# Performance work log

Measured on AMD Instinct MI355X. Metric: run time of the kernel, lower is better.

Reference implementation:

```python
import jax, jax.numpy as jnp
import numpy as np

B, S, D = 1, 2048, 2048      # batch, seq, hidden_dim
DF = 768                      # moe intermediate (per routed expert)
DSH = 2048                    # shared-expert intermediate
E, K = 32, 8                  # num routed experts, top_k
BLK = 128                     # fp8 block-scale size
CAP = 1024
T = B * S


def _dequant(w, s, blk=BLK):
    # w: [E, M, N] fp8 values (stored fp32), s: [E, M/blk, N/blk] block scales
    Eh, M, N = w.shape
    Mb, Nb = s.shape[1], s.shape[2]
    return (w.reshape(Eh, Mb, blk, Nb, blk) * s[:, :, None, :, None]).reshape(Eh, M, N)


def setup_inputs() -> dict:
    key = jax.random.key(0)
    ks = jax.random.split(key, 13)
    n = lambda k, shp, sc=0.02: jax.random.normal(k, shp, jnp.float32) * sc
    u = lambda k, shp: jax.random.uniform(k, shp, jnp.float32, 0.005, 0.02)
    return {
        "hidden_states": jax.random.normal(ks[0], (B, S, D), jnp.float32),
        "router_w": n(ks[1], (E, D)),
        # raw fp8-value weights (simulated as fp32 integers-in-range values) + block scale_inv
        "wg_fp8": jax.random.normal(ks[2], (E, DF, D), jnp.float32),
        "sg": u(ks[3], (E, DF // BLK, D // BLK)),
        "wu_fp8": jax.random.normal(ks[4], (E, DF, D), jnp.float32),
        "su": u(ks[5], (E, DF // BLK, D // BLK)),
        "wd_fp8": jax.random.normal(ks[6], (E, D, DF), jnp.float32),
        "sd": u(ks[7], (E, D // BLK, DF // BLK)),
        "ws_gate": n(ks[8], (DSH, D)),
        "ws_up": n(ks[9], (DSH, D)),
        "ws_down": n(ks[10], (D, DSH)),
        "w_shared_gate": n(ks[11], (1, D)),
    }


def reference(hidden_states, router_w, wg_fp8, sg, wu_fp8, su, wd_fp8, sd,
              ws_gate, ws_up, ws_down, w_shared_gate):
    x = hidden_states.reshape(-1, D)  # [T, D]

    # shared expert (SwiGLU) + its sigmoid gate
    shared = (jax.nn.silu(x @ ws_gate.T) * (x @ ws_up.T)) @ ws_down.T
    sh_gate = jax.nn.sigmoid(x @ w_shared_gate.T)  # [T, 1]

    # router: softmax -> top-k -> renormalize (Qwen MoE gate)
    probs = jax.nn.softmax(x @ router_w.T, axis=-1)          # [T, E]
    rw, sel = jax.lax.top_k(probs, K)                        # [T, K]
    rw = rw / jnp.sum(rw, axis=-1, keepdims=True)

    # capacity-based dispatch (replaces the python per-expert loop; same math)
    flat_e = sel.reshape(-1)                                 # [T*K]
    oh = jax.nn.one_hot(flat_e, E, dtype=jnp.int32)
    pos = jnp.sum(jnp.cumsum(oh, axis=0) * oh, axis=-1) - 1  # position within expert
    keep = (pos < CAP)
    pos_c = jnp.minimum(pos, CAP)                            # overflow -> scratch slot CAP
    tok = jnp.arange(T * K) // K                             # owning token of each (t,k) pair

    buf = jnp.zeros((E, CAP + 1, D), x.dtype).at[flat_e, pos_c].set(x[tok])

    # block-scale dequant (fp8*scale_inv), then per-expert SwiGLU
    Wg = _dequant(wg_fp8, sg)
    Wu = _dequant(wu_fp8, su)
    Wd = _dequant(wd_fp8, sd)
    g = jnp.einsum('ecd,efd->ecf', buf, Wg)
    up = jnp.einsum('ecd,efd->ecf', buf, Wu)
    h = jax.nn.silu(g) * up
    y = jnp.einsum('ecf,edf->ecd', h, Wd)                    # [E, CAP+1, D]

    # weighted scatter-add back to tokens (index_add_ equivalent)
    y_tok = y[flat_e, pos_c]                                 # [T*K, D]
    w_tok = rw.reshape(-1) * keep.astype(x.dtype)
    out = jax.ops.segment_sum(y_tok * w_tok[:, None], tok, num_segments=T)

    out = out + sh_gate * shared
    return out.reshape(B, S, D)
```

## Files before the change

### kernel.cpp

```cpp
#include <hip/hip_runtime.h>
#include <hip/hip_bf16.h>


#define TT   2048
#define DD   2048
#define DFF  768
#define DSH  2048
#define EE   32
#define KTOP 8
#define CAP  1024

typedef _Float16 half8  __attribute__((ext_vector_type(8)));
typedef _Float16 half4v __attribute__((ext_vector_type(4)));
typedef float    f32x4  __attribute__((ext_vector_type(4)));

__global__ __launch_bounds__(256) void k_init(int* __restrict__ cnt,
                                              int* __restrict__ slot_tok) {
  int i = blockIdx.x * 256 + threadIdx.x;
  if (i < EE * CAP) slot_tok[i] = 0;
  if (i < EE) cnt[i] = 0;
}

__global__ __launch_bounds__(256) void k_zero(float* __restrict__ out) {
  int i = blockIdx.x * 256 + threadIdx.x;
  ((float4*)out)[i] = (float4){0.f, 0.f, 0.f, 0.f};
}

__global__ __launch_bounds__(256) void k_cast(const float* __restrict__ in,
                                              _Float16* __restrict__ out) {
  int i = blockIdx.x * 256 + threadIdx.x;
  float4 v = ((const float4*)in)[i];
  half4v h = { (_Float16)v.x, (_Float16)v.y, (_Float16)v.z, (_Float16)v.w };
  ((half4v*)out)[i] = h;
}

__global__ __launch_bounds__(64) void k_router(
    const float* __restrict__ x, const float* __restrict__ rw,
    const float* __restrict__ wshg,
    float* __restrict__ shg, int* __restrict__ cnt,
    int* __restrict__ slot_tok, float* __restrict__ slot_w) {
  int t = blockIdx.x;
  int lane = threadIdx.x;
  const float* xr = x + (size_t)t * DD;
  float xv[32];
#pragma unroll
  for (int j = 0; j < 32; ++j) xv[j] = xr[lane + j * 64];

  __shared__ float lg[EE];
  for (int e = 0; e < EE; ++e) {
    const float* we = rw + (size_t)e * DD;
    float s = 0.f;
#pragma unroll
    for (int j = 0; j < 32; ++j) s += xv[j] * we[lane + j * 64];
#pragma unroll
    for (int off = 32; off > 0; off >>= 1) s += __shfl_down(s, off);
    if (lane == 0) lg[e] = s;
  }
  {
    float s = 0.f;
#pragma unroll
    for (int j = 0; j < 32; ++j) s += xv[j] * wshg[lane + j * 64];
#pragma unroll
    for (int off = 32; off > 0; off >>= 1) s += __shfl_down(s, off);
    if (lane == 0) shg[t] = 1.f / (1.f + expf(-s));
  }
  if (lane == 0) {
    unsigned used = 0;
    int sel[KTOP];
    float val[KTOP];
    for (int k = 0; k < KTOP; ++k) {
      float bv = -1e30f; int bi = 0;
      for (int e = 0; e < EE; ++e)
        if (!((used >> e) & 1) && lg[e] > bv) { bv = lg[e]; bi = e; }
      used |= (1u << bi);
      sel[k] = bi; val[k] = bv;
    }
    float mx = val[0], sum = 0.f;
    for (int k = 0; k < KTOP; ++k) { val[k] = expf(val[k] - mx); sum += val[k]; }
    float inv = 1.f / sum;
    for (int k = 0; k < KTOP; ++k) {
      int e = sel[k];
      int pos = atomicAdd(&cnt[e], 1);
      if (pos < CAP) {
        slot_tok[e * CAP + pos] = t;
        slot_w[e * CAP + pos] = val[k] * inv;
      }
    }
  }
}

template<bool DUAL, bool GATHER, bool DEQ, int EPI, int NPB, int MBB, int KDIM>
__global__ __launch_bounds__(256, 2) void k_gemm(
    const _Float16* __restrict__ A,
    const float* __restrict__ B0f, const float* __restrict__ B1f,
    const float* __restrict__ S0, const float* __restrict__ S1,
    int sCols, int sStrideE,
    _Float16* __restrict__ OutH, float* __restrict__ OutF,
    const float* __restrict__ shg,
    int ldA, int ldOut,
    long long strideAE, long long strideBE, long long strideOE,
    const int* __restrict__ cnt, int rowsConst,
    const int* __restrict__ slot_tok, const float* __restrict__ slot_w) {
  constexpr int BK = 64;
  constexpr int KT = KDIM / BK;
  constexpr int NF = DUAL ? 2 : 4;
  constexpr int BN = DUAL ? 64 : 128;
  constexpr int BCH = DUAL ? 4 : 8;

  const int f = blockIdx.x;
  const int xcd = f & 7;
  const int t0 = f >> 3;
  const int mb = t0 % MBB;
  const int pp = t0 / MBB;
  const int p  = pp * 8 + xcd;
  const int nb = p % NPB;
  const int e  = p / NPB;

  int rows = cnt ? (cnt[e] > CAP ? CAP : cnt[e]) : rowsConst;
  const int rowBase = mb * 128;
  if (rowBase >= rows) return;
  const int nBase = nb * BN;

  const int tid = threadIdx.x;
  const int lane = tid & 63;
  const int wave = tid >> 6;
  const int wr = wave >> 1;
  const int wc = wave & 1;

  __shared__ __align__(16) _Float16 sA[3][8192];
  __shared__ __align__(16) _Float16 sB[2][8192];

  const _Float16* Ae = A + (GATHER ? 0 : (long long)e * strideAE);
  const float* B0e = B0f + (long long)e * strideBE;
  const float* B1e = DUAL ? (B1f + (long long)e * strideBE) : nullptr;
  const float* S0e = DEQ ? (S0 + (long long)e * sStrideE) : nullptr;
  const float* S1e = (DEQ && DUAL) ? (S1 + (long long)e * sStrideE) : nullptr;
  const int sRow = DEQ ? (nBase >> 7) * sCols : 0;

  long long aByte[4];
#pragma unroll
  for (int i = 0; i < 4; ++i) {
    int c = tid + i * 256;
    int row = c >> 3;
    int colB = ((c & 7) << 4) ^ ((row & 7) << 4);
    int src = GATHER ? slot_tok[e * CAP + rowBase + row] : (rowBase + row);
    aByte[i] = (long long)src * (2LL * ldA) + colB;
  }
  long long bOff[BCH];
  int wByte[BCH];
#pragma unroll
  for (int i = 0; i < BCH; ++i) {
    int c = tid + i * 256;
    int rn = c >> 4;
    int c4 = (c & 15) << 2;
    bOff[i] = (long long)(nBase + rn) * KDIM + c4;
    wByte[i] = ((rn << 7) + (c4 << 1)) ^ ((rn & 7) << 4);
  }

  f32x4 accG[4][NF];
  f32x4 accU[DUAL ? 4 : 1][NF];
#pragma unroll
  for (int m = 0; m < 4; ++m)
#pragma unroll
    for (int n = 0; n < NF; ++n) {
      accG[m][n] = (f32x4){0.f, 0.f, 0.f, 0.f};
      if constexpr (DUAL) accU[m][n] = (f32x4){0.f, 0.f, 0.f, 0.f};
    }

  auto stageA = [&](int kt, int buf) {
#pragma unroll
    for (int i = 0; i < 4; ++i) {
      __builtin_amdgcn_global_load_lds(
          (const __attribute__((address_space(1))) void*)
              ((const char*)Ae + aByte[i] + kt * (BK * 2)),
          (__attribute__((address_space(3))) void*)&sA[buf][(size_t)(tid + i * 256) * 8],
          16, 0, 0);
    }
  };
  auto loadB = [&](int kt, float4 (&r0)[BCH], float4 (&r1)[BCH]) {
    const int ko = kt * BK;
#pragma unroll
    for (int i = 0; i < BCH; ++i) r0[i] = *(const float4*)(B0e + bOff[i] + ko);
    if constexpr (DUAL) {
#pragma unroll
      for (int i = 0; i < BCH; ++i) r1[i] = *(const float4*)(B1e + bOff[i] + ko);
    }
  };
  auto storeB = [&](int kt, float4 (&r0)[BCH], float4 (&r1)[BCH]) {
    float s0 = 1.f, s1 = 1.f;
    if constexpr (DEQ) {
      s0 = S0e[sRow + (kt >> 1)];
      if constexpr (DUAL) s1 = S1e[sRow + (kt >> 1)];
    }
    char* base = (char*)&sB[kt & 1][0];
#pragma unroll
    for (int i = 0; i < BCH; ++i) {
      half4v h = { (_Float16)(r0[i].x * s0), (_Float16)(r0[i].y * s0),
                   (_Float16)(r0[i].z * s0), (_Float16)(r0[i].w * s0) };
      *(half4v*)(base + wByte[i]) = h;
      if constexpr (DUAL) {
        half4v h1 = { (_Float16)(r1[i].x * s1), (_Float16)(r1[i].y * s1),
                      (_Float16)(r1[i].z * s1), (_Float16)(r1[i].w * s1) };
        *(half4v*)(base + 8192 + wByte[i]) = h1;
      }
    }
  };
  auto computeTile = [&](int ia, int ib) {
    const char* pA = (const char*)&sA[ia][0];
    const char* pB = (const char*)&sB[ib][0];
#pragma unroll
    for (int kk = 0; kk < 2; ++kk) {
      const int koff = kk * 32 + (lane >> 4) * 8;
      half8 a[4];
#pragma unroll
      for (int m = 0; m < 4; ++m) {
        int r = wr * 64 + m * 16 + (lane & 15);
        int byt = ((r << 7) + (koff << 1)) ^ ((r & 7) << 4);
        a[m] = *(const half8*)(pA + byt);
      }
      if constexpr (DUAL) {
        half8 bg[2], bu[2];
#pragma unroll
        for (int n = 0; n < 2; ++n) {
          int rn = wc * 32 + n * 16 + (lane & 15);
          int byt = ((rn << 7) + (koff << 1)) ^ ((rn & 7) << 4);
          bg[n] = *(const half8*)(pB + byt);
          bu[n] = *(const half8*)(pB + 8192 + byt);
        }
#pragma unroll
        for (int m = 0; m < 4; ++m)
#pragma unroll
          for (int n = 0; n < 2; ++n) {
            accG[m][n] = __builtin_amdgcn_mfma_f32_16x16x32_f16(a[m], bg[n], accG[m][n], 0, 0, 0);
            accU[m][n] = __builtin_amdgcn_mfma_f32_16x16x32_f16(a[m], bu[n], accU[m][n], 0, 0, 0);
          }
      } else {
        half8 b[4];
#pragma unroll
        for (int n = 0; n < 4; ++n) {
          int rn = wc * 64 + n * 16 + (lane & 15);
          int byt = ((rn << 7) + (koff << 1)) ^ ((rn & 7) << 4);
          b[n] = *(const half8*)(pB + byt);
        }
#pragma unroll
        for (int m = 0; m < 4; ++m)
#pragma unroll
          for (int n = 0; n < 4; ++n)
            accG[m][n] = __builtin_amdgcn_mfma_f32_16x16x32_f16(a[m], b[n], accG[m][n], 0, 0, 0);
      }
    }
  };

  float4 rbE0[BCH], rbE1[BCH], rbO0[BCH], rbO1[BCH];

  stageA(0, 0); loadB(0, rbE0, rbE1);
  __builtin_amdgcn_sched_barrier(0);
  stageA(1, 1); loadB(1, rbO0, rbO1);
  __builtin_amdgcn_sched_barrier(0);

  int bufC = 0;
  int bufW = 2;

  for (int kt = 0; kt < KT; kt += 2) {
    if (kt + 1 < KT) { asm volatile("s_waitcnt vmcnt(12)" ::: "memory"); }
    else             { asm volatile("s_waitcnt vmcnt(0)"  ::: "memory"); }
    __builtin_amdgcn_sched_barrier(0);
    storeB(kt, rbE0, rbE1);
    asm volatile("s_waitcnt lgkmcnt(0)" ::: "memory");
    __builtin_amdgcn_sched_barrier(0);
    __builtin_amdgcn_s_barrier();
    __builtin_amdgcn_sched_barrier(0);
    if (kt + 2 < KT) { stageA(kt + 2, bufW); loadB(kt + 2, rbE0, rbE1); }
    __builtin_amdgcn_sched_barrier(0);
    computeTile(bufC, 0);
    bufC = (bufC == 2) ? 0 : bufC + 1;
    bufW = (bufW == 2) ? 0 : bufW + 1;

    if (kt + 2 < KT) { asm volatile("s_waitcnt vmcnt(12)" ::: "memory"); }
    else             { asm volatile("s_waitcnt vmcnt(0)"  ::: "memory"); }
    __builtin_amdgcn_sched_barrier(0);
    storeB(kt + 1, rbO0, rbO1);
    asm volatile("s_waitcnt lgkmcnt(0)" ::: "memory");
    __builtin_amdgcn_sched_barrier(0);
    __builtin_amdgcn_s_barrier();
    __builtin_amdgcn_sched_barrier(0);
    if (kt + 3 < KT) { stageA(kt + 3, bufW); loadB(kt + 3, rbO0, rbO1); }
    __builtin_amdgcn_sched_barrier(0);
    computeTile(bufC, 1);
    bufC = (bufC == 2) ? 0 : bufC + 1;
    bufW = (bufW == 2) ? 0 : bufW + 1;
  }

#pragma unroll
  for (int m = 0; m < 4; ++m) {
#pragma unroll
    for (int i = 0; i < 4; ++i) {
      int row = rowBase + wr * 64 + m * 16 + (lane >> 4) * 4 + i;
      if (row < rows) {
        if constexpr (EPI == 1) {
          int tok = slot_tok[e * CAP + row];
          float w = slot_w[e * CAP + row];
#pragma unroll
          for (int n = 0; n < NF; ++n) {
            int col = nBase + wc * 64 + n * 16 + (lane & 15);
            unsafeAtomicAdd(&OutF[(long long)tok * DD + col], w * accG[m][n][i]);
          }
        } else if constexpr (EPI == 2) {
          float g = shg[row];
#pragma unroll
          for (int n = 0; n < NF; ++n) {
            int col = nBase + wc * 64 + n * 16 + (lane & 15);
            long long o = (long long)row * DD + col;
            OutF[o] += g * accG[m][n][i];
          }
        } else {
          long long outBase = (long long)e * strideOE;
#pragma unroll
          for (int n = 0; n < NF; ++n) {
            int col = nBase + (DUAL ? wc * 32 : wc * 64) + n * 16 + (lane & 15);
            long long o = outBase + (long long)row * ldOut + col;
            if constexpr (DUAL) {
              float gv = accG[m][n][i];
              float uv = accU[m][n][i];
              OutH[o] = (_Float16)((gv / (1.f + __expf(-gv))) * uv);
            } else {
              OutH[o] = (_Float16)accG[m][n][i];
            }
          }
        }
      }
    }
  }
}

extern "C" void kernel_launch(void* const* d_in, const int* in_sizes, int n_in,
                              void* d_out, int out_size, void* d_ws, size_t ws_size,
                              hipStream_t stream) {
  (void)in_sizes; (void)n_in; (void)out_size; (void)ws_size;
  const float* x    = (const float*)d_in[0];
  const float* rw   = (const float*)d_in[1];
  const float* wg   = (const float*)d_in[2];
  const float* sg   = (const float*)d_in[3];
  const float* wu   = (const float*)d_in[4];
  const float* su   = (const float*)d_in[5];
  const float* wd   = (const float*)d_in[6];
  const float* sd   = (const float*)d_in[7];
  const float* wsg  = (const float*)d_in[8];
  const float* wsu  = (const float*)d_in[9];
  const float* wsd  = (const float*)d_in[10];
  const float* wshg = (const float*)d_in[11];
  float* out = (float*)d_out;

  char* p = (char*)d_ws;
  auto alloc = [&](size_t bytes) {
    char* r = p;
    p += (bytes + 255) & ~(size_t)255;
    return r;
  };
  _Float16* x_h = (_Float16*)alloc((size_t)TT * DD * 2);
  _Float16* H   = (_Float16*)alloc((size_t)EE * CAP * DFF * 2);
  _Float16* Hsh = (_Float16*)alloc((size_t)TT * DSH * 2);
  float* shg    = (float*)alloc((size_t)TT * 4);
  int* cnt      = (int*)alloc((size_t)EE * 4);
  int* slot_tok = (int*)alloc((size_t)EE * CAP * 4);
  float* slot_w = (float*)alloc((size_t)EE * CAP * 4);

  k_init<<<(EE * CAP + 255) / 256, 256, 0, stream>>>(cnt, slot_tok);
  k_zero<<<(TT * DD / 4) / 256, 256, 0, stream>>>(out);
  k_cast<<<(TT * DD / 4) / 256, 256, 0, stream>>>(x, x_h);
  k_router<<<TT, 64, 0, stream>>>(x, rw, wshg, shg, cnt, slot_tok, slot_w);

  k_gemm<true, true, true, 0, 12, 8, DD><<<3072, 256, 0, stream>>>(
      x_h, wg, wu, sg, su, DD / 128, (DFF / 128) * (DD / 128),
      H, nullptr, nullptr,
      DD, DFF,
      0LL, (long long)DFF * DD, (long long)CAP * DFF,
      cnt, 0, slot_tok, nullptr);

  k_gemm<false, false, true, 1, 16, 8, DFF><<<4096, 256, 0, stream>>>(
      H, wd, wd, sd, sd, DFF / 128, (DD / 128) * (DFF / 128),
      nullptr, out, nullptr,
      DFF, DD,
      (long long)CAP * DFF, (long long)DD * DFF, 0LL,
      cnt, 0, slot_tok, slot_w);

  k_gemm<true, false, false, 0, 32, 16, DD><<<512, 256, 0, stream>>>(
      x_h, wsg, wsu, nullptr, nullptr, 0, 0,
      Hsh, nullptr, nullptr,
      DD, DSH,
      0LL, 0LL, 0LL,
      nullptr, TT, nullptr, nullptr);

  k_gemm<false, false, false, 2, 16, 16, DSH><<<256, 256, 0, stream>>>(
      Hsh, wsd, wsd, nullptr, nullptr, 0, 0,
      nullptr, out, shg,
      DSH, DD,
      0LL, 0LL, 0LL,
      nullptr, TT, nullptr, nullptr);
}
```

Measured before the change: 708.6 us.

## Use 512-thread 256-row GEMM tiles with phased LDS pipeline and cached scales

```diff
diff --git a/kernel.cpp b/kernel.cpp
--- a/kernel.cpp
+++ b/kernel.cpp
@@ -90,11 +90,11 @@
 }
 
 template<bool DUAL, bool GATHER, bool DEQ, int EPI, int NPB, int MBB, int KDIM>
-__global__ __launch_bounds__(256, 2) void k_gemm(
+__global__ __launch_bounds__(512, 2) void k_gemm(
     const _Float16* __restrict__ A,
     const float* __restrict__ B0f, const float* __restrict__ B1f,
     const float* __restrict__ S0, const float* __restrict__ S1,
-    int sCols, int sStrideE,
+    int sStrideE,
     _Float16* __restrict__ OutH, float* __restrict__ OutF,
     const float* __restrict__ shg,
     int ldA, int ldOut,
@@ -103,9 +103,8 @@
     const int* __restrict__ slot_tok, const float* __restrict__ slot_w) {
   constexpr int BK = 64;
   constexpr int KT = KDIM / BK;
-  constexpr int NF = DUAL ? 2 : 4;
-  constexpr int BN = DUAL ? 64 : 128;
-  constexpr int BCH = DUAL ? 4 : 8;
+  constexpr int KS = KDIM / 128;
+  constexpr int NFE = DUAL ? 1 : 2;
 
   const int f = blockIdx.x;
   const int xcd = f & 7;
@@ -117,215 +116,217 @@
   const int e  = p / NPB;
 
   int rows = cnt ? (cnt[e] > CAP ? CAP : cnt[e]) : rowsConst;
-  const int rowBase = mb * 128;
+  const int rowBase = mb * 256;
   if (rowBase >= rows) return;
-  const int nBase = nb * BN;
+  const int nBase = nb * (DUAL ? 64 : 128);
 
   const int tid = threadIdx.x;
   const int lane = tid & 63;
   const int wave = tid >> 6;
-  const int wr = wave >> 1;
-  const int wc = wave & 1;
-
-  __shared__ __align__(16) _Float16 sA[3][8192];
+  const int wr = wave >> 2;
+  const int wc = wave & 3;
+
+  __shared__ __align__(16) _Float16 sA[3][16384];
   __shared__ __align__(16) _Float16 sB[2][8192];
+  __shared__ float sSc[2][16];
 
   const _Float16* Ae = A + (GATHER ? 0 : (long long)e * strideAE);
   const float* B0e = B0f + (long long)e * strideBE;
   const float* B1e = DUAL ? (B1f + (long long)e * strideBE) : nullptr;
-  const float* S0e = DEQ ? (S0 + (long long)e * sStrideE) : nullptr;
-  const float* S1e = (DEQ && DUAL) ? (S1 + (long long)e * sStrideE) : nullptr;
-  const int sRow = DEQ ? (nBase >> 7) * sCols : 0;
-
-  long long aByte[4];
+
+  if constexpr (DEQ) {
+    const int sRow = (nBase >> 7) * KS;
+    if (tid < KS) sSc[0][tid] = S0[(long long)e * sStrideE + sRow + tid];
+    if (DUAL && tid >= 64 && tid < 64 + KS)
+      sSc[1][tid - 64] = S1[(long long)e * sStrideE + sRow + tid - 64];
+    __syncthreads();
+  }
+
+  int aByte[4];
 #pragma unroll
   for (int i = 0; i < 4; ++i) {
-    int c = tid + i * 256;
+    int c = tid + i * 512;
     int row = c >> 3;
     int colB = ((c & 7) << 4) ^ ((row & 7) << 4);
     int src = GATHER ? slot_tok[e * CAP + rowBase + row] : (rowBase + row);
-    aByte[i] = (long long)src * (2LL * ldA) + colB;
-  }
-  long long bOff[BCH];
-  int wByte[BCH];
-#pragma unroll
-  for (int i = 0; i < BCH; ++i) {
-    int c = tid + i * 256;
-    int rn = c >> 4;
-    int c4 = (c & 15) << 2;
-    bOff[i] = (long long)(nBase + rn) * KDIM + c4;
-    wByte[i] = ((rn << 7) + (c4 << 1)) ^ ((rn & 7) << 4);
-  }
-
-  f32x4 accG[4][NF];
-  f32x4 accU[DUAL ? 4 : 1][NF];
-#pragma unroll
-  for (int m = 0; m < 4; ++m)
-#pragma unroll
-    for (int n = 0; n < NF; ++n) {
-      accG[m][n] = (f32x4){0.f, 0.f, 0.f, 0.f};
-      if constexpr (DUAL) accU[m][n] = (f32x4){0.f, 0.f, 0.f, 0.f};
-    }
+    aByte[i] = src * (2 * ldA) + colB;
+  }
+  int bOff[4], wByte[4];
+#pragma unroll
+  for (int i = 0; i < 4; ++i) {
+    int c = tid + i * 512;
+    int rn = DUAL ? ((c & 1023) >> 4) : (c >> 4);
+    int c4 = (c & 15) * 4;
+    bOff[i] = (nBase + rn) * KDIM + c4;
+    wByte[i] = ((DUAL && i >= 2) ? 8192 : 0) +
+               ((((rn << 7) + (c4 << 1)) ^ ((rn & 7) << 4)));
+  }
+
+  f32x4 accG[8][NFE];
+  f32x4 accU[DUAL ? 8 : 1][1];
+#pragma unroll
+  for (int m = 0; m < 8; ++m) {
+#pragma unroll
+    for (int n = 0; n < NFE; ++n) accG[m][n] = (f32x4){0.f, 0.f, 0.f, 0.f};
+    if constexpr (DUAL) accU[m][0] = (f32x4){0.f, 0.f, 0.f, 0.f};
+  }
 
   auto stageA = [&](int kt, int buf) {
 #pragma unroll
     for (int i = 0; i < 4; ++i) {
       __builtin_amdgcn_global_load_lds(
           (const __attribute__((address_space(1))) void*)
-              ((const char*)Ae + aByte[i] + kt * (BK * 2)),
-          (__attribute__((address_space(3))) void*)&sA[buf][(size_t)(tid + i * 256) * 8],
+              ((const char*)Ae + (long long)aByte[i] + kt * 128),
+          (__attribute__((address_space(3))) void*)&sA[buf][(tid + i * 512) * 8],
           16, 0, 0);
     }
   };
-  auto loadB = [&](int kt, float4 (&r0)[BCH], float4 (&r1)[BCH]) {
+  auto loadB = [&](int kt, float4 (&r)[4]) {
     const int ko = kt * BK;
 #pragma unroll
-    for (int i = 0; i < BCH; ++i) r0[i] = *(const float4*)(B0e + bOff[i] + ko);
-    if constexpr (DUAL) {
-#pragma unroll
-      for (int i = 0; i < BCH; ++i) r1[i] = *(const float4*)(B1e + bOff[i] + ko);
+    for (int i = 0; i < 4; ++i) {
+      const float* src = (DUAL && i >= 2) ? B1e : B0e;
+      r[i] = *(const float4*)(src + bOff[i] + ko);
     }
   };
-  auto storeB = [&](int kt, float4 (&r0)[BCH], float4 (&r1)[BCH]) {
+  auto writeB = [&](int tw, float4 (&r)[4]) {
     float s0 = 1.f, s1 = 1.f;
     if constexpr (DEQ) {
-      s0 = S0e[sRow + (kt >> 1)];
-      if constexpr (DUAL) s1 = S1e[sRow + (kt >> 1)];
-    }
-    char* base = (char*)&sB[kt & 1][0];
-#pragma unroll
-    for (int i = 0; i < BCH; ++i) {
-      half4v h = { (_Float16)(r0[i].x * s0), (_Float16)(r0[i].y * s0),
-                   (_Float16)(r0[i].z * s0), (_Float16)(r0[i].w * s0) };
+      s0 = sSc[0][tw >> 1];
+      if constexpr (DUAL) s1 = sSc[1][tw >> 1];
+    }
+    char* base = (char*)&sB[0][0] + (tw & 1) * 16384;
+#pragma unroll
+    for (int i = 0; i < 4; ++i) {
+      float sc = (DUAL && i >= 2) ? s1 : s0;
+      half4v h = { (_Float16)(r[i].x * sc), (_Float16)(r[i].y * sc),
+                   (_Float16)(r[i].z * sc), (_Float16)(r[i].w * sc) };
       *(half4v*)(base + wByte[i]) = h;
-      if constexpr (DUAL) {
-        half4v h1 = { (_Float16)(r1[i].x * s1), (_Float16)(r1[i].y * s1),
-                      (_Float16)(r1[i].z * s1), (_Float16)(r1[i].w * s1) };
-        *(half4v*)(base + 8192 + wByte[i]) = h1;
-      }
     }
   };
-  auto computeTile = [&](int ia, int ib) {
-    const char* pA = (const char*)&sA[ia][0];
-    const char* pB = (const char*)&sB[ib][0];
-#pragma unroll
-    for (int kk = 0; kk < 2; ++kk) {
-      const int koff = kk * 32 + (lane >> 4) * 8;
-      half8 a[4];
-#pragma unroll
-      for (int m = 0; m < 4; ++m) {
-        int r = wr * 64 + m * 16 + (lane & 15);
-        int byt = ((r << 7) + (koff << 1)) ^ ((r & 7) << 4);
-        a[m] = *(const half8*)(pA + byt);
-      }
-      if constexpr (DUAL) {
-        half8 bg[2], bu[2];
-#pragma unroll
-        for (int n = 0; n < 2; ++n) {
-          int rn = wc * 32 + n * 16 + (lane & 15);
-          int byt = ((rn << 7) + (koff << 1)) ^ ((rn & 7) << 4);
-          bg[n] = *(const half8*)(pB + byt);
-          bu[n] = *(const half8*)(pB + 8192 + byt);
+
+  float4 rE[4], rO[4];
+
+  loadB(0, rE); stageA(0, 0);
+  loadB(1, rO); stageA(1, 1);
+  asm volatile("s_waitcnt vmcnt(12)" ::: "memory");
+  writeB(0, rE);
+  asm volatile("s_waitcnt lgkmcnt(0)" ::: "memory");
+  __builtin_amdgcn_sched_barrier(0);
+  __builtin_amdgcn_s_barrier();
+
+  const int koffB0 = (lane >> 4) * 16;
+
+  auto tile = [&](int t, int bufR, int bufD, float4 (&rIss)[4], float4 (&rWr)[4]) {
+    const char* pA = (const char*)&sA[0][0] + bufR * 32768;
+    const char* pB = (const char*)&sB[0][0] + (t & 1) * 16384;
+    half8 bg[2], bu[2], bs0[2], bs1[2];
+#pragma unroll
+    for (int ph = 0; ph < 4; ++ph) {
+      if (ph == 0) {
+        if (t + 2 < KT) loadB(t + 2, rIss);
+        if constexpr (DUAL) {
+          int rn = wc * 16 + (lane & 15);
+          int rb = rn << 7, sw = (rn & 7) << 4;
+          bg[0] = *(const half8*)(pB + ((rb + koffB0) ^ sw));
+          bg[1] = *(const half8*)(pB + ((rb + koffB0 + 64) ^ sw));
+          bu[0] = *(const half8*)(pB + 8192 + ((rb + koffB0) ^ sw));
+          bu[1] = *(const half8*)(pB + 8192 + ((rb + koffB0 + 64) ^ sw));
+        } else {
+          int rn0 = wc * 32 + (lane & 15);
+          int rb0 = rn0 << 7, sw0 = (rn0 & 7) << 4;
+          bs0[0] = *(const half8*)(pB + ((rb0 + koffB0) ^ sw0));
+          bs0[1] = *(const half8*)(pB + ((rb0 + koffB0 + 64) ^ sw0));
+          int rn1 = rn0 + 16;
+          int rb1 = rn1 << 7, sw1 = (rn1 & 7) << 4;
+          bs1[0] = *(const half8*)(pB + ((rb1 + koffB0) ^ sw1));
+          bs1[1] = *(const half8*)(pB + ((rb1 + koffB0 + 64) ^ sw1));
         }
-#pragma unroll
-        for (int m = 0; m < 4; ++m)
-#pragma unroll
-          for (int n = 0; n < 2; ++n) {
-            accG[m][n] = __builtin_amdgcn_mfma_f32_16x16x32_f16(a[m], bg[n], accG[m][n], 0, 0, 0);
-            accU[m][n] = __builtin_amdgcn_mfma_f32_16x16x32_f16(a[m], bu[n], accU[m][n], 0, 0, 0);
+      }
+      if (ph == 1 && t + 2 < KT) stageA(t + 2, bufD);
+      half8 a[2][2];
+#pragma unroll
+      for (int mm = 0; mm < 2; ++mm) {
+        int r = wr * 128 + (2 * ph + mm) * 16 + (lane & 15);
+        int rb = r << 7, sw = (r & 7) << 4;
+        a[mm][0] = *(const half8*)(pA + ((rb + koffB0) ^ sw));
+        a[mm][1] = *(const half8*)(pA + ((rb + koffB0 + 64) ^ sw));
+      }
+      if (ph == 3) {
+        if (t + 2 < KT) { asm volatile("s_waitcnt vmcnt(12)" ::: "memory"); }
+        else            { asm volatile("s_waitcnt vmcnt(0)"  ::: "memory"); }
+        if (t + 1 < KT) writeB(t + 1, rWr);
+      }
+      __builtin_amdgcn_s_barrier();
+      asm volatile("s_waitcnt lgkmcnt(0)" ::: "memory");
+      __builtin_amdgcn_sched_barrier(0);
+      __builtin_amdgcn_s_setprio(1);
+#pragma unroll
+      for (int mm = 0; mm < 2; ++mm) {
+#pragma unroll
+        for (int kk = 0; kk < 2; ++kk) {
+          if constexpr (DUAL) {
+            accG[2 * ph + mm][0] = __builtin_amdgcn_mfma_f32_16x16x32_f16(
+                a[mm][kk], bg[kk], accG[2 * ph + mm][0], 0, 0, 0);
+            accU[2 * ph + mm][0] = __builtin_amdgcn_mfma_f32_16x16x32_f16(
+                a[mm][kk], bu[kk], accU[2 * ph + mm][0], 0, 0, 0);
+          } else {
+            accG[2 * ph + mm][0] = __builtin_amdgcn_mfma_f32_16x16x32_f16(
+                a[mm][kk], bs0[kk], accG[2 * ph + mm][0], 0, 0, 0);
+            accG[2 * ph + mm][1] = __builtin_amdgcn_mfma_f32_16x16x32_f16(
+                a[mm][kk], bs1[kk], accG[2 * ph + mm][1], 0, 0, 0);
           }
-      } else {
-        half8 b[4];
-#pragma unroll
-        for (int n = 0; n < 4; ++n) {
-          int rn = wc * 64 + n * 16 + (lane & 15);
-          int byt = ((rn << 7) + (koff << 1)) ^ ((rn & 7) << 4);
-          b[n] = *(const half8*)(pB + byt);
         }
-#pragma unroll
-        for (int m = 0; m < 4; ++m)
-#pragma unroll
-          for (int n = 0; n < 4; ++n)
-            accG[m][n] = __builtin_amdgcn_mfma_f32_16x16x32_f16(a[m], b[n], accG[m][n], 0, 0, 0);
-      }
+      }
+      __builtin_amdgcn_s_setprio(0);
+      __builtin_amdgcn_sched_barrier(0);
+      __builtin_amdgcn_s_barrier();
     }
   };
 
-  float4 rbE0[BCH], rbE1[BCH], rbO0[BCH], rbO1[BCH];
-
-  stageA(0, 0); loadB(0, rbE0, rbE1);
-  __builtin_amdgcn_sched_barrier(0);
-  stageA(1, 1); loadB(1, rbO0, rbO1);
-  __builtin_amdgcn_sched_barrier(0);
-
-  int bufC = 0;
-  int bufW = 2;
-
-  for (int kt = 0; kt < KT; kt += 2) {
-    if (kt + 1 < KT) { asm volatile("s_waitcnt vmcnt(12)" ::: "memory"); }
-    else             { asm volatile("s_waitcnt vmcnt(0)"  ::: "memory"); }
-    __builtin_amdgcn_sched_barrier(0);
-    storeB(kt, rbE0, rbE1);
-    asm volatile("s_waitcnt lgkmcnt(0)" ::: "memory");
-    __builtin_amdgcn_sched_barrier(0);
-    __builtin_amdgcn_s_barrier();
-    __builtin_amdgcn_sched_barrier(0);
-    if (kt + 2 < KT) { stageA(kt + 2, bufW); loadB(kt + 2, rbE0, rbE1); }
-    __builtin_amdgcn_sched_barrier(0);
-    computeTile(bufC, 0);
-    bufC = (bufC == 2) ? 0 : bufC + 1;
-    bufW = (bufW == 2) ? 0 : bufW + 1;
-
-    if (kt + 2 < KT) { asm volatile("s_waitcnt vmcnt(12)" ::: "memory"); }
-    else             { asm volatile("s_waitcnt vmcnt(0)"  ::: "memory"); }
-    __builtin_amdgcn_sched_barrier(0);
-    storeB(kt + 1, rbO0, rbO1);
-    asm volatile("s_waitcnt lgkmcnt(0)" ::: "memory");
-    __builtin_amdgcn_sched_barrier(0);
-    __builtin_amdgcn_s_barrier();
-    __builtin_amdgcn_sched_barrier(0);
-    if (kt + 3 < KT) { stageA(kt + 3, bufW); loadB(kt + 3, rbO0, rbO1); }
-    __builtin_amdgcn_sched_barrier(0);
-    computeTile(bufC, 1);
-    bufC = (bufC == 2) ? 0 : bufC + 1;
-    bufW = (bufW == 2) ? 0 : bufW + 1;
-  }
-
-#pragma unroll
-  for (int m = 0; m < 4; ++m) {
+  int bufR = 0, bufD = 2;
+  for (int t2 = 0; t2 < KT; t2 += 2) {
+    tile(t2, bufR, bufD, rE, rO);
+    bufR = (bufR == 2) ? 0 : bufR + 1;
+    bufD = (bufD == 2) ? 0 : bufD + 1;
+    tile(t2 + 1, bufR, bufD, rO, rE);
+    bufR = (bufR == 2) ? 0 : bufR + 1;
+    bufD = (bufD == 2) ? 0 : bufD + 1;
+  }
+
+#pragma unroll
+  for (int m = 0; m < 8; ++m) {
 #pragma unroll
     for (int i = 0; i < 4; ++i) {
-      int row = rowBase + wr * 64 + m * 16 + (lane >> 4) * 4 + i;
+      int row = rowBase + wr * 128 + m * 16 + (lane >> 4) * 4 + i;
       if (row < rows) {
         if constexpr (EPI == 1) {
           int tok = slot_tok[e * CAP + row];
           float w = slot_w[e * CAP + row];
 #pragma unroll
-          for (int n = 0; n < NF; ++n) {
-            int col = nBase + wc * 64 + n * 16 + (lane & 15);
+          for (int n = 0; n < NFE; ++n) {
+            int col = nBase + wc * 32 + n * 16 + (lane & 15);
             unsafeAtomicAdd(&OutF[(long long)tok * DD + col], w * accG[m][n][i]);
           }
         } else if constexpr (EPI == 2) {
           float g = shg[row];
 #pragma unroll
-          for (int n = 0; n < NF; ++n) {
-            int col = nBase + wc * 64 + n * 16 + (lane & 15);
-            long long o = (long long)row * DD + col;
-            OutF[o] += g * accG[m][n][i];
+          for (int n = 0; n < NFE; ++n) {
+            int col = nBase + wc * 32 + n * 16 + (lane & 15);
+            OutF[(long long)row * DD + col] += g * accG[m][n][i];
           }
+        } else if constexpr (DUAL) {
+          int col = nBase + wc * 16 + (lane & 15);
+          float gv = accG[m][0][i];
+          float uv = accU[m][0][i];
+          OutH[(long long)e * strideOE + (long long)row * ldOut + col] =
+              (_Float16)((gv / (1.f + __expf(-gv))) * uv);
         } else {
-          long long outBase = (long long)e * strideOE;
-#pragma unroll
-          for (int n = 0; n < NF; ++n) {
-            int col = nBase + (DUAL ? wc * 32 : wc * 64) + n * 16 + (lane & 15);
-            long long o = outBase + (long long)row * ldOut + col;
-            if constexpr (DUAL) {
-              float gv = accG[m][n][i];
-              float uv = accU[m][n][i];
-              OutH[o] = (_Float16)((gv / (1.f + __expf(-gv))) * uv);
-            } else {
-              OutH[o] = (_Float16)accG[m][n][i];
-            }
+#pragma unroll
+          for (int n = 0; n < 2; ++n) {
+            int col = nBase + wc * 32 + n * 16 + (lane & 15);
+            OutH[(long long)e * strideOE + (long long)row * ldOut + col] =
+                (_Float16)accG[m][n][i];
           }
         }
       }
@@ -370,29 +371,29 @@
   k_cast<<<(TT * DD / 4) / 256, 256, 0, stream>>>(x, x_h);
   k_router<<<TT, 64, 0, stream>>>(x, rw, wshg, shg, cnt, slot_tok, slot_w);
 
-  k_gemm<true, true, true, 0, 12, 8, DD><<<3072, 256, 0, stream>>>(
-      x_h, wg, wu, sg, su, DD / 128, (DFF / 128) * (DD / 128),
+  k_gemm<true, true, true, 0, 12, 4, DD><<<1536, 512, 0, stream>>>(
+      x_h, wg, wu, sg, su, (DFF / 128) * (DD / 128),
       H, nullptr, nullptr,
       DD, DFF,
       0LL, (long long)DFF * DD, (long long)CAP * DFF,
       cnt, 0, slot_tok, nullptr);
 
-  k_gemm<false, false, true, 1, 16, 8, DFF><<<4096, 256, 0, stream>>>(
-      H, wd, wd, sd, sd, DFF / 128, (DD / 128) * (DFF / 128),
+  k_gemm<false, false, true, 1, 16, 4, DFF><<<2048, 512, 0, stream>>>(
+      H, wd, wd, sd, sd, (DD / 128) * (DFF / 128),
       nullptr, out, nullptr,
       DFF, DD,
       (long long)CAP * DFF, (long long)DD * DFF, 0LL,
       cnt, 0, slot_tok, slot_w);
 
-  k_gemm<true, false, false, 0, 32, 16, DD><<<512, 256, 0, stream>>>(
-      x_h, wsg, wsu, nullptr, nullptr, 0, 0,
+  k_gemm<true, false, false, 0, 32, 8, DD><<<256, 512, 0, stream>>>(
+      x_h, wsg, wsu, nullptr, nullptr, 0,
       Hsh, nullptr, nullptr,
       DD, DSH,
       0LL, 0LL, 0LL,
       nullptr, TT, nullptr, nullptr);
 
-  k_gemm<false, false, false, 2, 16, 16, DSH><<<256, 256, 0, stream>>>(
-      Hsh, wsd, wsd, nullptr, nullptr, 0, 0,
+  k_gemm<false, false, false, 2, 16, 8, DSH><<<128, 512, 0, stream>>>(
+      Hsh, wsd, wsd, nullptr, nullptr, 0,
       nullptr, out, shg,
       DSH, DD,
       0LL, 0LL, 0LL,
```

After: 980.0 us. 1.38x slower.

## Deepen B-weight register prefetch to three stages and preload block scales to LDS

Applied to the files above, without the earlier changes.

```diff
diff --git a/kernel.cpp b/kernel.cpp
--- a/kernel.cpp
+++ b/kernel.cpp
@@ -94,7 +94,7 @@
     const _Float16* __restrict__ A,
     const float* __restrict__ B0f, const float* __restrict__ B1f,
     const float* __restrict__ S0, const float* __restrict__ S1,
-    int sCols, int sStrideE,
+    int sStrideE,
     _Float16* __restrict__ OutH, float* __restrict__ OutF,
     const float* __restrict__ shg,
     int ldA, int ldOut,
@@ -103,6 +103,7 @@
     const int* __restrict__ slot_tok, const float* __restrict__ slot_w) {
   constexpr int BK = 64;
   constexpr int KT = KDIM / BK;
+  constexpr int KS = KDIM / 128;
   constexpr int NF = DUAL ? 2 : 4;
   constexpr int BN = DUAL ? 64 : 128;
   constexpr int BCH = DUAL ? 4 : 8;
@@ -129,31 +130,36 @@
 
   __shared__ __align__(16) _Float16 sA[3][8192];
   __shared__ __align__(16) _Float16 sB[2][8192];
+  __shared__ float sSc[2][16];
 
   const _Float16* Ae = A + (GATHER ? 0 : (long long)e * strideAE);
   const float* B0e = B0f + (long long)e * strideBE;
   const float* B1e = DUAL ? (B1f + (long long)e * strideBE) : nullptr;
-  const float* S0e = DEQ ? (S0 + (long long)e * sStrideE) : nullptr;
-  const float* S1e = (DEQ && DUAL) ? (S1 + (long long)e * sStrideE) : nullptr;
-  const int sRow = DEQ ? (nBase >> 7) * sCols : 0;
-
-  long long aByte[4];
+
+  if constexpr (DEQ) {
+    const int sRow = (nBase >> 7) * KS;
+    if (tid < KS) sSc[0][tid] = S0[(long long)e * sStrideE + sRow + tid];
+    if (DUAL && tid >= 64 && tid < 64 + KS)
+      sSc[1][tid - 64] = S1[(long long)e * sStrideE + sRow + tid - 64];
+    __syncthreads();
+  }
+
+  int aByte[4];
 #pragma unroll
   for (int i = 0; i < 4; ++i) {
     int c = tid + i * 256;
     int row = c >> 3;
     int colB = ((c & 7) << 4) ^ ((row & 7) << 4);
     int src = GATHER ? slot_tok[e * CAP + rowBase + row] : (rowBase + row);
-    aByte[i] = (long long)src * (2LL * ldA) + colB;
-  }
-  long long bOff[BCH];
-  int wByte[BCH];
+    aByte[i] = src * (2 * ldA) + colB;
+  }
+  int bOff[BCH], wByte[BCH];
 #pragma unroll
   for (int i = 0; i < BCH; ++i) {
     int c = tid + i * 256;
     int rn = c >> 4;
     int c4 = (c & 15) << 2;
-    bOff[i] = (long long)(nBase + rn) * KDIM + c4;
+    bOff[i] = (nBase + rn) * KDIM + c4;
     wByte[i] = ((rn << 7) + (c4 << 1)) ^ ((rn & 7) << 4);
   }
 
@@ -173,7 +179,7 @@
       __builtin_amdgcn_global_load_lds(
           (const __attribute__((address_space(1))) void*)
               ((const char*)Ae + aByte[i] + kt * (BK * 2)),
-          (__attribute__((address_space(3))) void*)&sA[buf][(size_t)(tid + i * 256) * 8],
+          (__attribute__((address_space(3))) void*)&sA[buf][(tid + i * 256) * 8],
           16, 0, 0);
     }
   };
@@ -186,12 +192,8 @@
       for (int i = 0; i < BCH; ++i) r1[i] = *(const float4*)(B1e + bOff[i] + ko);
     }
   };
-  auto storeB = [&](int kt, float4 (&r0)[BCH], float4 (&r1)[BCH]) {
-    float s0 = 1.f, s1 = 1.f;
-    if constexpr (DEQ) {
-      s0 = S0e[sRow + (kt >> 1)];
-      if constexpr (DUAL) s1 = S1e[sRow + (kt >> 1)];
-    }
+  auto storeB = [&](int kt, float s0, float s1,
+                    float4 (&r0)[BCH], float4 (&r1)[BCH]) {
     char* base = (char*)&sB[kt & 1][0];
 #pragma unroll
     for (int i = 0; i < BCH; ++i) {
@@ -251,44 +253,46 @@
     }
   };
 
-  float4 rbE0[BCH], rbE1[BCH], rbO0[BCH], rbO1[BCH];
-
-  stageA(0, 0); loadB(0, rbE0, rbE1);
+  float4 rA0[BCH], rA1[BCH], rB0[BCH], rB1[BCH], rC0[BCH], rC1[BCH];
+
+  stageA(0, 0);
   __builtin_amdgcn_sched_barrier(0);
-  stageA(1, 1); loadB(1, rbO0, rbO1);
+  loadB(0, rA0, rA1);
   __builtin_amdgcn_sched_barrier(0);
-
-  int bufC = 0;
-  int bufW = 2;
-
-  for (int kt = 0; kt < KT; kt += 2) {
-    if (kt + 1 < KT) { asm volatile("s_waitcnt vmcnt(12)" ::: "memory"); }
-    else             { asm volatile("s_waitcnt vmcnt(0)"  ::: "memory"); }
+  stageA(1, 1);
+  __builtin_amdgcn_sched_barrier(0);
+  loadB(1, rB0, rB1);
+  __builtin_amdgcn_sched_barrier(0);
+  loadB(2, rC0, rC1);
+  __builtin_amdgcn_sched_barrier(0);
+
+  auto step = [&](int t, float4 (&r0)[BCH], float4 (&r1)[BCH],
+                  int bufR, int bufW) {
+    float s0 = 1.f, s1 = 1.f;
+    if constexpr (DEQ) {
+      s0 = sSc[0][t >> 1];
+      if constexpr (DUAL) s1 = sSc[1][t >> 1];
+    }
+    asm volatile("s_waitcnt vmcnt(20)" ::: "memory");
     __builtin_amdgcn_sched_barrier(0);
-    storeB(kt, rbE0, rbE1);
+    storeB(t, s0, s1, r0, r1);
     asm volatile("s_waitcnt lgkmcnt(0)" ::: "memory");
     __builtin_amdgcn_sched_barrier(0);
     __builtin_amdgcn_s_barrier();
     __builtin_amdgcn_sched_barrier(0);
-    if (kt + 2 < KT) { stageA(kt + 2, bufW); loadB(kt + 2, rbE0, rbE1); }
+    int ta = (t + 2 < KT) ? t + 2 : KT - 1;
+    int tb = (t + 3 < KT) ? t + 3 : KT - 1;
+    stageA(ta, bufW);
     __builtin_amdgcn_sched_barrier(0);
-    computeTile(bufC, 0);
-    bufC = (bufC == 2) ? 0 : bufC + 1;
-    bufW = (bufW == 2) ? 0 : bufW + 1;
-
-    if (kt + 2 < KT) { asm volatile("s_waitcnt vmcnt(12)" ::: "memory"); }
-    else             { asm volatile("s_waitcnt vmcnt(0)"  ::: "memory"); }
+    loadB(tb, r0, r1);
     __builtin_amdgcn_sched_barrier(0);
-    storeB(kt + 1, rbO0, rbO1);
-    asm volatile("s_waitcnt lgkmcnt(0)" ::: "memory");
-    __builtin_amdgcn_sched_barrier(0);
-    __builtin_amdgcn_s_barrier();
-    __builtin_amdgcn_sched_barrier(0);
-    if (kt + 3 < KT) { stageA(kt + 3, bufW); loadB(kt + 3, rbO0, rbO1); }
-    __builtin_amdgcn_sched_barrier(0);
-    computeTile(bufC, 1);
-    bufC = (bufC == 2) ? 0 : bufC + 1;
-    bufW = (bufW == 2) ? 0 : bufW + 1;
+    computeTile(bufR, t & 1);
+  };
+
+  for (int kt = 0; kt < KT; kt += 3) {
+    step(kt, rA0, rA1, 0, 2);
+    if (kt + 1 < KT) step(kt + 1, rB0, rB1, 1, 0);
+    if (kt + 2 < KT) step(kt + 2, rC0, rC1, 2, 1);
   }
 
 #pragma unroll
@@ -371,28 +375,28 @@
   k_router<<<TT, 64, 0, stream>>>(x, rw, wshg, shg, cnt, slot_tok, slot_w);
 
   k_gemm<true, true, true, 0, 12, 8, DD><<<3072, 256, 0, stream>>>(
-      x_h, wg, wu, sg, su, DD / 128, (DFF / 128) * (DD / 128),
+      x_h, wg, wu, sg, su, (DFF / 128) * (DD / 128),
       H, nullptr, nullptr,
       DD, DFF,
       0LL, (long long)DFF * DD, (long long)CAP * DFF,
       cnt, 0, slot_tok, nullptr);
 
   k_gemm<false, false, true, 1, 16, 8, DFF><<<4096, 256, 0, stream>>>(
-      H, wd, wd, sd, sd, DFF / 128, (DD / 128) * (DFF / 128),
+      H, wd, wd, sd, sd, (DD / 128) * (DFF / 128),
       nullptr, out, nullptr,
       DFF, DD,
       (long long)CAP * DFF, (long long)DD * DFF, 0LL,
       cnt, 0, slot_tok, slot_w);
 
   k_gemm<true, false, false, 0, 32, 16, DD><<<512, 256, 0, stream>>>(
-      x_h, wsg, wsu, nullptr, nullptr, 0, 0,
+      x_h, wsg, wsu, nullptr, nullptr, 0,
       Hsh, nullptr, nullptr,
       DD, DSH,
       0LL, 0LL, 0LL,
       nullptr, TT, nullptr, nullptr);
 
   k_gemm<false, false, false, 2, 16, 16, DSH><<<256, 256, 0, stream>>>(
-      Hsh, wsd, wsd, nullptr, nullptr, 0, 0,
+      Hsh, wsd, wsd, nullptr, nullptr, 0,
       nullptr, out, shg,
       DSH, DD,
       0LL, 0LL, 0LL,
```

New measurement: 956.3 us. 35.0% more time.

## Replace atomic scatter-add with per-pair fp16 buffer and deterministic combine kernel

Applied to the files above, without the earlier changes.

```diff
diff --git a/kernel.cpp b/kernel.cpp
--- a/kernel.cpp
+++ b/kernel.cpp
@@ -21,11 +21,6 @@
   if (i < EE) cnt[i] = 0;
 }
 
-__global__ __launch_bounds__(256) void k_zero(float* __restrict__ out) {
-  int i = blockIdx.x * 256 + threadIdx.x;
-  ((float4*)out)[i] = (float4){0.f, 0.f, 0.f, 0.f};
-}
-
 __global__ __launch_bounds__(256) void k_cast(const float* __restrict__ in,
                                               _Float16* __restrict__ out) {
   int i = blockIdx.x * 256 + threadIdx.x;
@@ -38,7 +33,8 @@
     const float* __restrict__ x, const float* __restrict__ rw,
     const float* __restrict__ wshg,
     float* __restrict__ shg, int* __restrict__ cnt,
-    int* __restrict__ slot_tok, float* __restrict__ slot_w) {
+    int* __restrict__ slot_tok, float* __restrict__ slot_w,
+    int* __restrict__ slot_pair, int* __restrict__ pair_pos) {
   int t = blockIdx.x;
   int lane = threadIdx.x;
   const float* xr = x + (size_t)t * DD;
@@ -81,9 +77,11 @@
     for (int k = 0; k < KTOP; ++k) {
       int e = sel[k];
       int pos = atomicAdd(&cnt[e], 1);
+      pair_pos[t * KTOP + k] = pos;
       if (pos < CAP) {
         slot_tok[e * CAP + pos] = t;
         slot_w[e * CAP + pos] = val[k] * inv;
+        slot_pair[e * CAP + pos] = t * KTOP + k;
       }
     }
   }
@@ -137,23 +135,22 @@
   const float* S1e = (DEQ && DUAL) ? (S1 + (long long)e * sStrideE) : nullptr;
   const int sRow = DEQ ? (nBase >> 7) * sCols : 0;
 
-  long long aByte[4];
+  int aByte[4];
 #pragma unroll
   for (int i = 0; i < 4; ++i) {
     int c = tid + i * 256;
     int row = c >> 3;
     int colB = ((c & 7) << 4) ^ ((row & 7) << 4);
     int src = GATHER ? slot_tok[e * CAP + rowBase + row] : (rowBase + row);
-    aByte[i] = (long long)src * (2LL * ldA) + colB;
-  }
-  long long bOff[BCH];
-  int wByte[BCH];
+    aByte[i] = src * (2 * ldA) + colB;
+  }
+  int bOff[BCH], wByte[BCH];
 #pragma unroll
   for (int i = 0; i < BCH; ++i) {
     int c = tid + i * 256;
     int rn = c >> 4;
     int c4 = (c & 15) << 2;
-    bOff[i] = (long long)(nBase + rn) * KDIM + c4;
+    bOff[i] = (nBase + rn) * KDIM + c4;
     wByte[i] = ((rn << 7) + (c4 << 1)) ^ ((rn & 7) << 4);
   }
 
@@ -173,7 +170,7 @@
       __builtin_amdgcn_global_load_lds(
           (const __attribute__((address_space(1))) void*)
               ((const char*)Ae + aByte[i] + kt * (BK * 2)),
-          (__attribute__((address_space(3))) void*)&sA[buf][(size_t)(tid + i * 256) * 8],
+          (__attribute__((address_space(3))) void*)&sA[buf][(tid + i * 256) * 8],
           16, 0, 0);
     }
   };
@@ -298,12 +295,12 @@
       int row = rowBase + wr * 64 + m * 16 + (lane >> 4) * 4 + i;
       if (row < rows) {
         if constexpr (EPI == 1) {
-          int tok = slot_tok[e * CAP + row];
+          int pair = slot_tok[e * CAP + row];
           float w = slot_w[e * CAP + row];
 #pragma unroll
           for (int n = 0; n < NF; ++n) {
             int col = nBase + wc * 64 + n * 16 + (lane & 15);
-            unsafeAtomicAdd(&OutF[(long long)tok * DD + col], w * accG[m][n][i]);
+            OutH[(long long)pair * DD + col] = (_Float16)(w * accG[m][n][i]);
           }
         } else if constexpr (EPI == 2) {
           float g = shg[row];
@@ -331,6 +328,26 @@
       }
     }
   }
+}
+
+__global__ __launch_bounds__(256) void k_combine(
+    const _Float16* __restrict__ Yp, const int* __restrict__ pair_pos,
+    float* __restrict__ out) {
+  int t = blockIdx.x;
+  int col = threadIdx.x * 8;
+  float acc[8] = {0.f, 0.f, 0.f, 0.f, 0.f, 0.f, 0.f, 0.f};
+#pragma unroll
+  for (int k = 0; k < KTOP; ++k) {
+    if (pair_pos[t * KTOP + k] < CAP) {
+      half8 y = *(const half8*)&Yp[((size_t)t * KTOP + k) * DD + col];
+#pragma unroll
+      for (int j = 0; j < 8; ++j) acc[j] += (float)y[j];
+    }
+  }
+  float4 o0 = {acc[0], acc[1], acc[2], acc[3]};
+  float4 o1 = {acc[4], acc[5], acc[6], acc[7]};
+  *(float4*)&out[(size_t)t * DD + col] = o0;
+  *(float4*)&out[(size_t)t * DD + col + 4] = o1;
 }
 
 extern "C" void kernel_launch(void* const* d_in, const int* in_sizes, int n_in,
@@ -357,18 +374,21 @@
     p += (bytes + 255) & ~(size_t)255;
     return r;
   };
-  _Float16* x_h = (_Float16*)alloc((size_t)TT * DD * 2);
-  _Float16* H   = (_Float16*)alloc((size_t)EE * CAP * DFF * 2);
-  _Float16* Hsh = (_Float16*)alloc((size_t)TT * DSH * 2);
-  float* shg    = (float*)alloc((size_t)TT * 4);
-  int* cnt      = (int*)alloc((size_t)EE * 4);
-  int* slot_tok = (int*)alloc((size_t)EE * CAP * 4);
-  float* slot_w = (float*)alloc((size_t)EE * CAP * 4);
+  _Float16* x_h   = (_Float16*)alloc((size_t)TT * DD * 2);
+  _Float16* H     = (_Float16*)alloc((size_t)EE * CAP * DFF * 2);
+  _Float16* Hsh   = (_Float16*)alloc((size_t)TT * DSH * 2);
+  _Float16* Yp    = (_Float16*)alloc((size_t)TT * KTOP * DD * 2);
+  float* shg      = (float*)alloc((size_t)TT * 4);
+  int* cnt        = (int*)alloc((size_t)EE * 4);
+  int* slot_tok   = (int*)alloc((size_t)EE * CAP * 4);
+  float* slot_w   = (float*)alloc((size_t)EE * CAP * 4);
+  int* slot_pair  = (int*)alloc((size_t)EE * CAP * 4);
+  int* pair_pos   = (int*)alloc((size_t)TT * KTOP * 4);
 
   k_init<<<(EE * CAP + 255) / 256, 256, 0, stream>>>(cnt, slot_tok);
-  k_zero<<<(TT * DD / 4) / 256, 256, 0, stream>>>(out);
   k_cast<<<(TT * DD / 4) / 256, 256, 0, stream>>>(x, x_h);
-  k_router<<<TT, 64, 0, stream>>>(x, rw, wshg, shg, cnt, slot_tok, slot_w);
+  k_router<<<TT, 64, 0, stream>>>(x, rw, wshg, shg, cnt, slot_tok, slot_w,
+                                  slot_pair, pair_pos);
 
   k_gemm<true, true, true, 0, 12, 8, DD><<<3072, 256, 0, stream>>>(
       x_h, wg, wu, sg, su, DD / 128, (DFF / 128) * (DD / 128),
@@ -379,10 +399,12 @@
 
   k_gemm<false, false, true, 1, 16, 8, DFF><<<4096, 256, 0, stream>>>(
       H, wd, wd, sd, sd, DFF / 128, (DD / 128) * (DFF / 128),
-      nullptr, out, nullptr,
+      Yp, nullptr, nullptr,
       DFF, DD,
       (long long)CAP * DFF, (long long)DD * DFF, 0LL,
-      cnt, 0, slot_tok, slot_w);
+      cnt, 0, slot_pair, slot_w);
+
+  k_combine<<<TT, 256, 0, stream>>>(Yp, pair_pos, out);
 
   k_gemm<true, false, false, 0, 32, 16, DD><<<512, 256, 0, stream>>>(
       x_h, wsg, wsu, nullptr, nullptr, 0, 0,
```

Result: faster. 680.4 us, median of 2 (-4.0%).
